# Performance work log

Hardware: AMD Instinct MI355X
Metric: run time of the kernel (lower is better)

Reference implementation:

```python
import jax, jax.numpy as jnp
import numpy as np
from jax import lax

NPOINT = 1024
K = 32
EPS = 1e-5  # BatchNorm eps (eval mode, running stats)


def _fps(xyz, npoint):
    """Farthest point sampling. xyz: [B,N,3] -> idx [B,npoint] (int32).
    Deterministic start at index 0 (torch version starts at a random index)."""
    B, N, _ = xyz.shape
    barange = jnp.arange(B)

    def step(carry, _):
        distance, farthest = carry
        centroid = xyz[barange, farthest]                    # [B,3]
        d = jnp.sum((xyz - centroid[:, None, :]) ** 2, -1)   # [B,N]
        distance = jnp.minimum(distance, d)
        new_far = jnp.argmax(distance, axis=-1).astype(jnp.int32)
        return (distance, new_far), farthest

    init = (jnp.full((B, N), 1e10, dtype=xyz.dtype), jnp.zeros((B,), jnp.int32))
    _, centroids = lax.scan(step, init, None, length=npoint)  # [npoint,B]
    return centroids.T                                        # [B,npoint]


def _square_distance(src, dst):
    # src [B,M,3], dst [B,N,3] -> [B,M,N]
    return (jnp.sum(src ** 2, -1)[:, :, None]
            - 2.0 * jnp.einsum('bmc,bnc->bmn', src, dst)
            + jnp.sum(dst ** 2, -1)[:, None, :])


def _gather(p, idx):
    # p [B,N,C], idx [B,...] -> [B,...,C]
    return jax.vmap(lambda pb, ib: pb[ib])(p, idx)


def _mlp_layer(x, w, cb, g, b, m, v):
    # x [B,S,K,Cin]; Conv2d 1x1 == channel matmul, then eval-mode BN, ReLU
    x = jnp.einsum('bskc,oc->bsko', x, w) + cb
    x = (x - m) * (g / jnp.sqrt(v + EPS)) + b
    return jax.nn.relu(x)


def _forward(xyz, points, w0, cb0, g0, b0, m0, v0,
             w1, cb1, g1, b1, m1, v1, w2, cb2, g2, b2, m2, v2):
    fps_idx = _fps(xyz, NPOINT)                       # [B,S]
    new_xyz = _gather(xyz, fps_idx)                   # [B,S,3]
    dists = _square_distance(new_xyz, xyz)            # [B,S,N]
    _, nn_idx = lax.top_k(-dists, K)                  # [B,S,K]
    grouped_xyz = _gather(xyz, nn_idx)                # [B,S,K,3]
    grouped_xyz_norm = grouped_xyz - new_xyz[:, :, None, :]
    grouped_pts = _gather(points, nn_idx)             # [B,S,K,C]
    x = jnp.concatenate([grouped_xyz_norm, grouped_pts], axis=-1)  # [B,S,K,3+C]
    x = _mlp_layer(x, w0, cb0, g0, b0, m0, v0)
    x = _mlp_layer(x, w1, cb1, g1, b1, m1, v1)
    x = _mlp_layer(x, w2, cb2, g2, b2, m2, v2)
    new_points = jnp.max(x, axis=2)                   # max over K -> [B,S,Cout]
    return new_xyz, jnp.transpose(new_points, (0, 2, 1))  # [B,Cout,S]


def setup_inputs() -> dict:
    key = jax.random.key(0)
    ks = jax.random.split(key, 8)
    B, N, C = 16, 4096, 64
    inp = {
        'xyz': jax.random.normal(ks[0], (B, N, 3), jnp.float32),
        'points': jax.random.normal(ks[1], (B, N, C), jnp.float32),
    }
    channels = [(3 + C, 64), (64, 64), (64, 128)]
    for li, (ci, co) in enumerate(channels):
        inp[f'w{li}'] = jax.random.normal(ks[2 + li], (co, ci), jnp.float32) * 0.05
        inp[f'cb{li}'] = jnp.zeros((co,), jnp.float32)
        inp[f'g{li}'] = jnp.ones((co,), jnp.float32)
        inp[f'b{li}'] = jnp.zeros((co,), jnp.float32)
        inp[f'm{li}'] = jnp.zeros((co,), jnp.float32)
        inp[f'v{li}'] = jnp.ones((co,), jnp.float32)
    return inp


def reference(xyz, points, w0, cb0, g0, b0, m0, v0,
              w1, cb1, g1, b1, m1, v1, w2, cb2, g2, b2, m2, v2):
    return _forward(xyz, points, w0, cb0, g0, b0, m0, v0,
                    w1, cb1, g1, b1, m1, v1, w2, cb2, g2, b2, m2, v2)
```

## Files before the change

### kernel.cpp

```cpp
#include <hip/hip_runtime.h>
#include <math.h>

#pragma clang fp contract(off)

#define NPTS 4096
#define NB 16
#define NS 1024
#define KNB 32
#define CPTS 64

#define FLAG_OFF_B  0
#define CNT_OFF_B   64
#define PUBC_OFF_B  128
#define WFRAG_ELEMS 18432
#define NUNITS      16384
#define CAP         256
#define GRAB        2

typedef __attribute__((ext_vector_type(8))) short short8;
typedef __attribute__((ext_vector_type(4))) float f32x4;
typedef __attribute__((ext_vector_type(2))) float f32x2;

__device__ __forceinline__ short f2bf(float f) {
  unsigned u = __float_as_uint(f);
  unsigned r = (u + 0x7fffu + ((u >> 16) & 1u)) >> 16;
  return (short)r;
}

template <int CTRL>
__device__ __forceinline__ int dppmov(int cur) {
  return __builtin_amdgcn_update_dpp(cur, cur, CTRL, 0xF, 0xF, false);
}
template <int CTRL>
__device__ __forceinline__ double dpp_fmax64(double x) {
  int hi = __double2hiint(x), lo = __double2loint(x);
  double o = __hiloint2double(dppmov<CTRL>(hi), dppmov<CTRL>(lo));
  return fmax(x, o);
}
__device__ __forceinline__ double mkkey(float d, unsigned lo) {
  return __hiloint2double((int)__float_as_uint(d), (int)lo);
}

#define XSTR 104
__global__ __launch_bounds__(512, 1) void fused_kernel(
    const float* __restrict__ xyz, const float* __restrict__ points,
    const float* __restrict__ w0, const float* __restrict__ cb0, const float* __restrict__ g0,
    const float* __restrict__ b0, const float* __restrict__ m0, const float* __restrict__ v0,
    const float* __restrict__ w1, const float* __restrict__ cb1, const float* __restrict__ g1,
    const float* __restrict__ b1, const float* __restrict__ m1, const float* __restrict__ v1,
    const float* __restrict__ w2, const float* __restrict__ cb2, const float* __restrict__ g2,
    const float* __restrict__ b2, const float* __restrict__ m2, const float* __restrict__ v2,
    char* __restrict__ wsb, float* __restrict__ newxyz, float* __restrict__ outp) {
  struct FpsSh {
    float4 sxyz4[NPTS];
    float4 centL[NS];
    unsigned long long part[2][8];
  };
  struct WorkerSh {
    short Wlds[WFRAG_ELEMS];
    short X[8][32 * XSTR];
    unsigned long long cand[8][CAP];
    int nnL[8][KNB];
    float biasL[256];
    unsigned cnt[8];
  };
  __shared__ union { FpsSh f; WorkerSh w; } sh;

  const int t = threadIdx.x;
  const int lane = t & 63;
  const int wave = t >> 6;
  unsigned* flagp = (unsigned*)(wsb + FLAG_OFF_B);
  unsigned* cntp  = (unsigned*)(wsb + CNT_OFF_B);
  float* pubC = (float*)(wsb + PUBC_OFF_B);

  if (blockIdx.x < NB) {
    const int b = blockIdx.x;
    const float* xb = xyz + (size_t)b * NPTS * 3;
    float* outb = newxyz + (size_t)b * NS * 3;

    for (int i = t; i < NPTS; i += 512)
      sh.f.sxyz4[i] = make_float4(xb[i * 3 + 0], xb[i * 3 + 1], xb[i * 3 + 2], 0.f);

    f32x2 px2[8], py2[8], pz2[8], d2[8];
    unsigned lo16[16];
    if (wave < 4) {
#pragma unroll
      for (int j = 0; j < 16; ++j) lo16[j] = ~(unsigned)(t + 256 * j);
#pragma unroll
      for (int j2 = 0; j2 < 8; ++j2) {
        int n0 = t + 512 * j2, n1 = t + 512 * j2 + 256;
        px2[j2].x = xb[n0 * 3 + 0]; px2[j2].y = xb[n1 * 3 + 0];
        py2[j2].x = xb[n0 * 3 + 1]; py2[j2].y = xb[n1 * 3 + 1];
        pz2[j2].x = xb[n0 * 3 + 2]; pz2[j2].y = xb[n1 * 3 + 2];
        d2[j2].x = 1e10f; d2[j2].y = 1e10f;
      }
    }
    __syncthreads();
    float cx = sh.f.sxyz4[0].x, cy = sh.f.sxyz4[0].y, cz = sh.f.sxyz4[0].z;
    if (t == 0) sh.f.centL[0] = sh.f.sxyz4[0];

    for (int it = 1; it < NS; ++it) {
      const int buf = it & 1;
      if (wave < 4) {
        f32x2 cax; cax.x = cx; cax.y = cx;
        f32x2 cay; cay.x = cy; cay.y = cy;
        f32x2 caz; caz.x = cz; caz.y = cz;
        double tt[8];
#pragma unroll
        for (int j2 = 0; j2 < 8; ++j2) {
          f32x2 dx = px2[j2] - cax;
          f32x2 dy = py2[j2] - cay;
          f32x2 dz = pz2[j2] - caz;
          f32x2 dd = (dx * dx + dy * dy) + dz * dz;
          f32x2 dv = d2[j2];
          dv.x = fminf(dv.x, dd.x);
          dv.y = fminf(dv.y, dd.y);
          d2[j2] = dv;
          tt[j2] = fmax(mkkey(dv.x, lo16[2 * j2]), mkkey(dv.y, lo16[2 * j2 + 1]));
        }
        double km = fmax(fmax(fmax(tt[0], tt[1]), fmax(tt[2], tt[3])),
                         fmax(fmax(tt[4], tt[5]), fmax(tt[6], tt[7])));
        km = dpp_fmax64<0xB1>(km);  km = dpp_fmax64<0x4E>(km);  km = dpp_fmax64<0x141>(km);
        km = dpp_fmax64<0x140>(km); km = dpp_fmax64<0x142>(km); km = dpp_fmax64<0x143>(km);
        if (lane == 63)
          sh.f.part[buf][wave] = (unsigned long long)__double_as_longlong(km);
      }
      __syncthreads();
      if (wave < 4) {
        double kw = __longlong_as_double((long long)sh.f.part[buf][lane & 3]);
        kw = dpp_fmax64<0xB1>(kw); kw = dpp_fmax64<0x4E>(kw);
        int bi = (int)(~(unsigned)__double2loint(kw)) & 4095;
        float4 c4 = sh.f.sxyz4[bi];
        cx = c4.x; cy = c4.y; cz = c4.z;
        if (t == 0) sh.f.centL[it] = c4;
        if ((it & 31) == 31 && wave == 0) {
          if (lane == 0) {
            asm volatile("s_waitcnt vmcnt(0)" ::: "memory");
            __hip_atomic_store(&flagp[b], (unsigned)(it - 31), __ATOMIC_RELAXED, __HIP_MEMORY_SCOPE_AGENT);
          }
          if (lane < 32) {
            int ci = it - 31 + lane;
            float4 cc = sh.f.centL[ci];
            float* dst = pubC + ((size_t)b * NS + ci) * 3;
            __hip_atomic_store(dst + 0, cc.x, __ATOMIC_RELAXED, __HIP_MEMORY_SCOPE_AGENT);
            __hip_atomic_store(dst + 1, cc.y, __ATOMIC_RELAXED, __HIP_MEMORY_SCOPE_AGENT);
            __hip_atomic_store(dst + 2, cc.z, __ATOMIC_RELAXED, __HIP_MEMORY_SCOPE_AGENT);
          }
        }
      }
    }
    if (wave == 0 && lane == 0) {
      asm volatile("s_waitcnt vmcnt(0)" ::: "memory");
      __hip_atomic_store(&flagp[b], (unsigned)NS, __ATOMIC_RELAXED, __HIP_MEMORY_SCOPE_AGENT);
    }
    __syncthreads();
    const float* cf = (const float*)sh.f.centL;
    for (int i = t; i < NS * 3; i += 512) {
      int p = i / 3, c = i - p * 3;
      outb[i] = cf[p * 4 + c];
    }
  }

  __syncthreads();
  for (int i = t; i < WFRAG_ELEMS; i += 512) {
    int g = i >> 9, ln = (i >> 3) & 63, j = i & 7;
    int l, nt, s;
    if (g < 12)      { l = 0; nt = g / 3;  s = g % 3; }
    else if (g < 20) { l = 1; int gg = g - 12; nt = gg >> 1; s = gg & 1; }
    else             { l = 2; int gg = g - 20; nt = gg >> 1; s = gg & 1; }
    int n = nt * 16 + (ln & 15);
    int k = s * 32 + ((ln >> 4) << 3) + j;
    float val = 0.f;
    if (l == 0) {
      float sc = g0[n] / sqrtf(v0[n] + 1e-5f);
      if (k < 64)      val = w0[n * 67 + (k + 3)] * sc;
      else if (k < 67) val = w0[n * 67 + (k - 64)] * sc;
    }
    else if (l == 1) { val = w1[n * 64 + k] * (g1[n] / sqrtf(v1[n] + 1e-5f)); }
    else { val = w2[n * 64 + k] * (g2[n] / sqrtf(v2[n] + 1e-5f)); }
    sh.w.Wlds[i] = f2bf(val);
  }
  if (t < 256) {
    int o = t;
    float bv;
    if (o < 64)       { float sc = g0[o] / sqrtf(v0[o] + 1e-5f); bv = (cb0[o] - m0[o]) * sc + b0[o]; }
    else if (o < 128) { int c = o - 64;  float sc = g1[c] / sqrtf(v1[c] + 1e-5f); bv = (cb1[c] - m1[c]) * sc + b1[c]; }
    else              { int c = o - 128; float sc = g2[c] / sqrtf(v2[c] + 1e-5f); bv = (cb2[c] - m2[c]) * sc + b2[c]; }
    sh.w.biasL[o] = bv;
  }
  __syncthreads();

  unsigned long long* cand = sh.w.cand[wave];
  for (int i = lane; i < (32 * XSTR) / 2; i += 64) ((int*)sh.w.X[wave])[i] = 0;

  unsigned fcache = 0;

  for (;;) {
    unsigned base = 0;
    if (lane == 0) base = atomicAdd(cntp, (unsigned)GRAB);
    base = (unsigned)__builtin_amdgcn_readfirstlane((int)base);
    if (base >= NUNITS) break;
    unsigned uend = base + GRAB;
    if (uend > NUNITS) uend = NUNITS;

    for (unsigned u = base; u < uend; ++u) {
    const int b = (int)(u & 15u);
    const int s = (int)(u >> 4);

    {
      unsigned need = (unsigned)s + 1u;
      unsigned have = (unsigned)__shfl((int)fcache, b, 64);
      if (have < need) {
        unsigned f;
        for (;;) {
          f = __hip_atomic_load(&flagp[b], __ATOMIC_RELAXED, __HIP_MEMORY_SCOPE_AGENT);
          if (f >= need) break;
          __builtin_amdgcn_s_sleep(64);
        }
        if (lane == b) fcache = f;
        asm volatile("" ::: "memory");
      }
    }
    const float* qcp = pubC + ((size_t)b * NS + s) * 3;
    float qx = __hip_atomic_load(qcp + 0, __ATOMIC_RELAXED, __HIP_MEMORY_SCOPE_AGENT);
    float qy = __hip_atomic_load(qcp + 1, __ATOMIC_RELAXED, __HIP_MEMORY_SCOPE_AGENT);
    float qz = __hip_atomic_load(qcp + 2, __ATOMIC_RELAXED, __HIP_MEMORY_SCOPE_AGENT);

    const float* xb = xyz + (size_t)b * NPTS * 3;
    float s2 = __fadd_rn(__fadd_rn(__fmul_rn(qx, qx), __fmul_rn(qy, qy)), __fmul_rn(qz, qz));

    unsigned long long mkey = 0xFFFFFFFFFFFFFFFFull;
#pragma unroll 4
    for (int j = 0; j < 64; ++j) {
      int n = j * 64 + lane;
      float px = xb[n * 3], py = xb[n * 3 + 1], pz = xb[n * 3 + 2];
      float n2 = __fadd_rn(__fadd_rn(__fmul_rn(px, px), __fmul_rn(py, py)), __fmul_rn(pz, pz));
      float dt = __fadd_rn(__fadd_rn(__fmul_rn(qx, px), __fmul_rn(qy, py)), __fmul_rn(qz, pz));
      float d  = __fadd_rn(__fsub_rn(s2, __fmul_rn(2.0f, dt)), n2);
      unsigned uu = __float_as_uint(d);
      uu ^= (0x80000000u | (unsigned)((int)uu >> 31));
      unsigned long long key = ((unsigned long long)uu << 32) | (unsigned)n;
      mkey = key < mkey ? key : mkey;
    }

    {
      unsigned mh = (unsigned)(mkey >> 32), ml2 = (unsigned)mkey;
#pragma unroll
      for (int k = 2; k <= 64; k <<= 1) {
#pragma unroll
        for (int j = k >> 1; j >= 1; j >>= 1) {
          unsigned oh = (unsigned)__shfl_xor((int)mh, j, 64);
          unsigned ol = (unsigned)__shfl_xor((int)ml2, j, 64);
          bool up = (lane & k) == 0;
          bool lower = (lane & j) == 0;
          bool omin = (oh < mh) || (oh == mh && ol < ml2);
          bool keep_o = (lower == up) ? omin : !omin;
          mh = keep_o ? oh : mh;
          ml2 = keep_o ? ol : ml2;
        }
      }
      unsigned th = (unsigned)__builtin_amdgcn_readlane((int)mh, 31);
      unsigned tl = (unsigned)__builtin_amdgcn_readlane((int)ml2, 31);
      mkey = ((unsigned long long)th << 32) | tl;
    }
    const unsigned long long tau = mkey;

    if (lane == 0) sh.w.cnt[wave] = 0;
    asm volatile("s_waitcnt lgkmcnt(0)" ::: "memory");
#pragma unroll 4
    for (int j = 0; j < 64; ++j) {
      int n = j * 64 + lane;
      float px = xb[n * 3], py = xb[n * 3 + 1], pz = xb[n * 3 + 2];
      float n2 = __fadd_rn(__fadd_rn(__fmul_rn(px, px), __fmul_rn(py, py)), __fmul_rn(pz, pz));
      float dt = __fadd_rn(__fadd_rn(__fmul_rn(qx, px), __fmul_rn(qy, py)), __fmul_rn(qz, pz));
      float d  = __fadd_rn(__fsub_rn(s2, __fmul_rn(2.0f, dt)), n2);
      unsigned uu = __float_as_uint(d);
      uu ^= (0x80000000u | (unsigned)((int)uu >> 31));
      unsigned long long key = ((unsigned long long)uu << 32) | (unsigned)n;
      if (key <= tau) {
        unsigned pos = atomicAdd(&sh.w.cnt[wave], 1u);
        if (pos < CAP) cand[pos] = key;
      }
    }
    asm volatile("s_waitcnt lgkmcnt(0)" ::: "memory");
    unsigned cn = sh.w.cnt[wave];
    if (cn > CAP) cn = CAP;

    for (unsigned bb = 0; bb < cn; bb += 64) {
      unsigned i = bb + (unsigned)lane;
      unsigned long long ki = (i < cn) ? cand[i] : 0xFFFFFFFFFFFFFFFFull;
      int rank = 0;
#pragma unroll 4
      for (unsigned c2 = 0; c2 < cn; ++c2)
        rank += (cand[c2] < ki) ? 1 : 0;
      if (i < cn && rank < KNB) sh.w.nnL[wave][rank] = (int)(unsigned)(ki & 0xFFFFFFFFull);
    }
    asm volatile("s_waitcnt lgkmcnt(0)" ::: "memory");

    {
      const int qi = wave;
      const float* pb = points + (size_t)b * NPTS * CPTS;
      const float* bias = sh.w.biasL;
      short* X = sh.w.X[qi];

      {
        int h = lane & 1, r = lane >> 1;
        int idx = sh.w.nnL[qi][r];
        const f32x4* src = (const f32x4*)(pb + (size_t)idx * CPTS) + h * 8;
        short8* dst = (short8*)&X[r * XSTR + h * 32];
#pragma unroll
        for (int q = 0; q < 4; ++q) {
          f32x4 v0 = src[q * 2], v1 = src[q * 2 + 1];
          short8 o;
          o[0] = f2bf(v0[0]); o[1] = f2bf(v0[1]); o[2] = f2bf(v0[2]); o[3] = f2bf(v0[3]);
          o[4] = f2bf(v1[0]); o[5] = f2bf(v1[1]); o[6] = f2bf(v1[2]); o[7] = f2bf(v1[3]);
          dst[q] = o;
        }
      }
      if (lane < 32) {
        int idx = sh.w.nnL[qi][lane];
        X[lane * XSTR + 64] = f2bf(__fsub_rn(xb[idx * 3 + 0], qx));
        X[lane * XSTR + 65] = f2bf(__fsub_rn(xb[idx * 3 + 1], qy));
        X[lane * XSTR + 66] = f2bf(__fsub_rn(xb[idx * 3 + 2], qz));
      }

      const int ml = lane & 15, quad = lane >> 4;
      const short8* Wf = (const short8*)sh.w.Wlds;

      short8 a0[2][3];
#pragma unroll
      for (int m2 = 0; m2 < 2; ++m2)
#pragma unroll
        for (int s3 = 0; s3 < 3; ++s3)
          a0[m2][s3] = *(const short8*)&X[(m2 * 16 + ml) * XSTR + s3 * 32 + quad * 8];
      f32x4 acc0[2][4];
#pragma unroll
      for (int m2 = 0; m2 < 2; ++m2)
#pragma unroll
        for (int nt = 0; nt < 4; ++nt) {
          f32x4 c = {0.f, 0.f, 0.f, 0.f};
#pragma unroll
          for (int s3 = 0; s3 < 3; ++s3)
            c = __builtin_amdgcn_mfma_f32_16x16x32_bf16(a0[m2][s3], Wf[(nt * 3 + s3) * 64 + lane], c, 0, 0, 0);
          acc0[m2][nt] = c;
        }
#pragma unroll
      for (int m2 = 0; m2 < 2; ++m2)
#pragma unroll
        for (int nt = 0; nt < 4; ++nt) {
          int ch = nt * 16 + ml;
          float bv = bias[ch];
#pragma unroll
          for (int r4 = 0; r4 < 4; ++r4) {
            float y = fmaxf(acc0[m2][nt][r4] + bv, 0.f);
            int m = quad * 4 + r4;
            int sK = ch >> 5, qq = (ch >> 3) & 3, jj = ch & 7;
            X[((m2 * 2 + sK) * 64 + qq * 16 + m) * 8 + jj] = f2bf(y);
          }
        }

      short8 a1[2][2];
#pragma unroll
      for (int m2 = 0; m2 < 2; ++m2)
#pragma unroll
        for (int sK = 0; sK < 2; ++sK)
          a1[m2][sK] = *(const short8*)&X[((m2 * 2 + sK) * 64 + lane) * 8];
      f32x4 acc1[2][4];
#pragma unroll
      for (int m2 = 0; m2 < 2; ++m2)
#pragma unroll
        for (int nt = 0; nt < 4; ++nt) {
          f32x4 c = {0.f, 0.f, 0.f, 0.f};
#pragma unroll
          for (int sK = 0; sK < 2; ++sK)
            c = __builtin_amdgcn_mfma_f32_16x16x32_bf16(a1[m2][sK], Wf[(12 + nt * 2 + sK) * 64 + lane], c, 0, 0, 0);
          acc1[m2][nt] = c;
        }
#pragma unroll
      for (int m2 = 0; m2 < 2; ++m2)
#pragma unroll
        for (int nt = 0; nt < 4; ++nt) {
          int ch = nt * 16 + ml;
          float bv = bias[64 + ch];
#pragma unroll
          for (int r4 = 0; r4 < 4; ++r4) {
            float y = fmaxf(acc1[m2][nt][r4] + bv, 0.f);
            int m = quad * 4 + r4;
            int sK = ch >> 5, qq = (ch >> 3) & 3, jj = ch & 7;
            X[((m2 * 2 + sK) * 64 + qq * 16 + m) * 8 + jj] = f2bf(y);
          }
        }

      short8 a2[2][2];
#pragma unroll
      for (int m2 = 0; m2 < 2; ++m2)
#pragma unroll
        for (int sK = 0; sK < 2; ++sK)
          a2[m2][sK] = *(const short8*)&X[((m2 * 2 + sK) * 64 + lane) * 8];
#pragma unroll
      for (int nt = 0; nt < 8; ++nt) {
        f32x4 c0 = {0.f, 0.f, 0.f, 0.f}, c1 = {0.f, 0.f, 0.f, 0.f};
        short8 w0f = Wf[(20 + nt * 2 + 0) * 64 + lane];
        short8 w1f = Wf[(20 + nt * 2 + 1) * 64 + lane];
        c0 = __builtin_amdgcn_mfma_f32_16x16x32_bf16(a2[0][0], w0f, c0, 0, 0, 0);
        c0 = __builtin_amdgcn_mfma_f32_16x16x32_bf16(a2[0][1], w1f, c0, 0, 0, 0);
        c1 = __builtin_amdgcn_mfma_f32_16x16x32_bf16(a2[1][0], w0f, c1, 0, 0, 0);
        c1 = __builtin_amdgcn_mfma_f32_16x16x32_bf16(a2[1][1], w1f, c1, 0, 0, 0);
        float bv = bias[128 + nt * 16 + ml];
        float m = -1.f;
#pragma unroll
        for (int r4 = 0; r4 < 4; ++r4) {
          m = fmaxf(m, fmaxf(c0[r4] + bv, 0.f));
          m = fmaxf(m, fmaxf(c1[r4] + bv, 0.f));
        }
        m = fmaxf(m, __shfl_xor(m, 16, 64));
        m = fmaxf(m, __shfl_xor(m, 32, 64));
        if (lane < 16) outp[((size_t)b * 128 + nt * 16 + lane) * NS + s] = m;
      }
    }
    }
  }
}

extern "C" void kernel_launch(void* const* d_in, const int* in_sizes, int n_in,
                              void* d_out, int out_size, void* d_ws, size_t ws_size,
                              hipStream_t stream) {
  const float* xyz    = (const float*)d_in[0];
  const float* points = (const float*)d_in[1];
  const float* w0  = (const float*)d_in[2];
  const float* cb0 = (const float*)d_in[3];
  const float* g0  = (const float*)d_in[4];
  const float* b0  = (const float*)d_in[5];
  const float* m0  = (const float*)d_in[6];
  const float* v0  = (const float*)d_in[7];
  const float* w1  = (const float*)d_in[8];
  const float* cb1 = (const float*)d_in[9];
  const float* g1  = (const float*)d_in[10];
  const float* b1  = (const float*)d_in[11];
  const float* m1  = (const float*)d_in[12];
  const float* v1  = (const float*)d_in[13];
  const float* w2  = (const float*)d_in[14];
  const float* cb2 = (const float*)d_in[15];
  const float* g2  = (const float*)d_in[16];
  const float* b2  = (const float*)d_in[17];
  const float* m2  = (const float*)d_in[18];
  const float* v2  = (const float*)d_in[19];

  char*  wsb    = (char*)d_ws;
  float* newxyz = (float*)d_out;
  float* outp   = (float*)d_out + (size_t)NB * NS * 3;

  hipMemsetAsync(wsb, 0, 128, stream);
  fused_kernel<<<256, 512, 0, stream>>>(
      xyz, points, w0, cb0, g0, b0, m0, v0, w1, cb1, g1, b1, m1, v1,
      w2, cb2, g2, b2, m2, v2, wsb, newxyz, outp);
}
```

Before: 901.8 us.

## Pack two FPS batch chains per block and relax launch bounds to two blocks

```diff
diff --git a/kernel.cpp b/kernel.cpp
--- a/kernel.cpp
+++ b/kernel.cpp
@@ -16,6 +16,7 @@
 #define NUNITS      16384
 #define CAP         256
 #define GRAB        2
+#define NFPSB       8
 
 typedef __attribute__((ext_vector_type(8))) short short8;
 typedef __attribute__((ext_vector_type(4))) float f32x4;
@@ -42,7 +43,7 @@
 }
 
 #define XSTR 104
-__global__ __launch_bounds__(512, 1) void fused_kernel(
+__global__ __launch_bounds__(512, 2) void fused_kernel(
     const float* __restrict__ xyz, const float* __restrict__ points,
     const float* __restrict__ w0, const float* __restrict__ cb0, const float* __restrict__ g0,
     const float* __restrict__ b0, const float* __restrict__ m0, const float* __restrict__ v0,
@@ -52,8 +53,8 @@
     const float* __restrict__ b2, const float* __restrict__ m2, const float* __restrict__ v2,
     char* __restrict__ wsb, float* __restrict__ newxyz, float* __restrict__ outp) {
   struct FpsSh {
-    float4 sxyz4[NPTS];
-    float4 centL[NS];
+    float4 sxyz4[2][NPTS];
+    float  centL[2][NS * 3];
     unsigned long long part[2][8];
   };
   struct WorkerSh {
@@ -73,91 +74,92 @@
   unsigned* cntp  = (unsigned*)(wsb + CNT_OFF_B);
   float* pubC = (float*)(wsb + PUBC_OFF_B);
 
-  if (blockIdx.x < NB) {
-    const int b = blockIdx.x;
+  if (blockIdx.x < NFPSB) {
+    const int chain = wave >> 2;
+    const int wc = wave & 3;
+    const int tc = wc * 64 + lane;
+    const int b = (int)blockIdx.x * 2 + chain;
     const float* xb = xyz + (size_t)b * NPTS * 3;
-    float* outb = newxyz + (size_t)b * NS * 3;
-
-    for (int i = t; i < NPTS; i += 512)
-      sh.f.sxyz4[i] = make_float4(xb[i * 3 + 0], xb[i * 3 + 1], xb[i * 3 + 2], 0.f);
+    float4* sx = sh.f.sxyz4[chain];
+    float* cL = sh.f.centL[chain];
+
+    for (int i = tc; i < NPTS; i += 256)
+      sx[i] = make_float4(xb[i * 3 + 0], xb[i * 3 + 1], xb[i * 3 + 2], 0.f);
 
     f32x2 px2[8], py2[8], pz2[8], d2[8];
     unsigned lo16[16];
-    if (wave < 4) {
-#pragma unroll
-      for (int j = 0; j < 16; ++j) lo16[j] = ~(unsigned)(t + 256 * j);
-#pragma unroll
-      for (int j2 = 0; j2 < 8; ++j2) {
-        int n0 = t + 512 * j2, n1 = t + 512 * j2 + 256;
-        px2[j2].x = xb[n0 * 3 + 0]; px2[j2].y = xb[n1 * 3 + 0];
-        py2[j2].x = xb[n0 * 3 + 1]; py2[j2].y = xb[n1 * 3 + 1];
-        pz2[j2].x = xb[n0 * 3 + 2]; pz2[j2].y = xb[n1 * 3 + 2];
-        d2[j2].x = 1e10f; d2[j2].y = 1e10f;
-      }
+#pragma unroll
+    for (int j = 0; j < 16; ++j) lo16[j] = ~(unsigned)(tc + 256 * j);
+#pragma unroll
+    for (int j2 = 0; j2 < 8; ++j2) {
+      int n0 = tc + 512 * j2, n1 = n0 + 256;
+      px2[j2].x = xb[n0 * 3 + 0]; px2[j2].y = xb[n1 * 3 + 0];
+      py2[j2].x = xb[n0 * 3 + 1]; py2[j2].y = xb[n1 * 3 + 1];
+      pz2[j2].x = xb[n0 * 3 + 2]; pz2[j2].y = xb[n1 * 3 + 2];
+      d2[j2].x = 1e10f; d2[j2].y = 1e10f;
     }
     __syncthreads();
-    float cx = sh.f.sxyz4[0].x, cy = sh.f.sxyz4[0].y, cz = sh.f.sxyz4[0].z;
-    if (t == 0) sh.f.centL[0] = sh.f.sxyz4[0];
+    float4 c4 = sx[0];
+    float cx = c4.x, cy = c4.y, cz = c4.z;
+    if (wc == 0 && lane == 0) { cL[0] = cx; cL[1] = cy; cL[2] = cz; }
 
     for (int it = 1; it < NS; ++it) {
       const int buf = it & 1;
-      if (wave < 4) {
-        f32x2 cax; cax.x = cx; cax.y = cx;
-        f32x2 cay; cay.x = cy; cay.y = cy;
-        f32x2 caz; caz.x = cz; caz.y = cz;
-        double tt[8];
-#pragma unroll
-        for (int j2 = 0; j2 < 8; ++j2) {
-          f32x2 dx = px2[j2] - cax;
-          f32x2 dy = py2[j2] - cay;
-          f32x2 dz = pz2[j2] - caz;
-          f32x2 dd = (dx * dx + dy * dy) + dz * dz;
-          f32x2 dv = d2[j2];
-          dv.x = fminf(dv.x, dd.x);
-          dv.y = fminf(dv.y, dd.y);
-          d2[j2] = dv;
-          tt[j2] = fmax(mkkey(dv.x, lo16[2 * j2]), mkkey(dv.y, lo16[2 * j2 + 1]));
-        }
-        double km = fmax(fmax(fmax(tt[0], tt[1]), fmax(tt[2], tt[3])),
-                         fmax(fmax(tt[4], tt[5]), fmax(tt[6], tt[7])));
-        km = dpp_fmax64<0xB1>(km);  km = dpp_fmax64<0x4E>(km);  km = dpp_fmax64<0x141>(km);
-        km = dpp_fmax64<0x140>(km); km = dpp_fmax64<0x142>(km); km = dpp_fmax64<0x143>(km);
-        if (lane == 63)
-          sh.f.part[buf][wave] = (unsigned long long)__double_as_longlong(km);
-      }
+      f32x2 cax; cax.x = cx; cax.y = cx;
+      f32x2 cay; cay.x = cy; cay.y = cy;
+      f32x2 caz; caz.x = cz; caz.y = cz;
+      double tt[8];
+#pragma unroll
+      for (int j2 = 0; j2 < 8; ++j2) {
+        f32x2 dx = px2[j2] - cax;
+        f32x2 dy = py2[j2] - cay;
+        f32x2 dz = pz2[j2] - caz;
+        f32x2 dd = (dx * dx + dy * dy) + dz * dz;
+        f32x2 dv = d2[j2];
+        dv.x = fminf(dv.x, dd.x);
+        dv.y = fminf(dv.y, dd.y);
+        d2[j2] = dv;
+        tt[j2] = fmax(mkkey(dv.x, lo16[2 * j2]), mkkey(dv.y, lo16[2 * j2 + 1]));
+      }
+      double km = fmax(fmax(fmax(tt[0], tt[1]), fmax(tt[2], tt[3])),
+                       fmax(fmax(tt[4], tt[5]), fmax(tt[6], tt[7])));
+      km = dpp_fmax64<0xB1>(km);  km = dpp_fmax64<0x4E>(km);  km = dpp_fmax64<0x141>(km);
+      km = dpp_fmax64<0x140>(km); km = dpp_fmax64<0x142>(km); km = dpp_fmax64<0x143>(km);
+      if (lane == 63)
+        sh.f.part[buf][wave] = (unsigned long long)__double_as_longlong(km);
       __syncthreads();
-      if (wave < 4) {
-        double kw = __longlong_as_double((long long)sh.f.part[buf][lane & 3]);
-        kw = dpp_fmax64<0xB1>(kw); kw = dpp_fmax64<0x4E>(kw);
-        int bi = (int)(~(unsigned)__double2loint(kw)) & 4095;
-        float4 c4 = sh.f.sxyz4[bi];
-        cx = c4.x; cy = c4.y; cz = c4.z;
-        if (t == 0) sh.f.centL[it] = c4;
-        if ((it & 31) == 31 && wave == 0) {
-          if (lane == 0) {
-            asm volatile("s_waitcnt vmcnt(0)" ::: "memory");
-            __hip_atomic_store(&flagp[b], (unsigned)(it - 31), __ATOMIC_RELAXED, __HIP_MEMORY_SCOPE_AGENT);
-          }
-          if (lane < 32) {
-            int ci = it - 31 + lane;
-            float4 cc = sh.f.centL[ci];
-            float* dst = pubC + ((size_t)b * NS + ci) * 3;
-            __hip_atomic_store(dst + 0, cc.x, __ATOMIC_RELAXED, __HIP_MEMORY_SCOPE_AGENT);
-            __hip_atomic_store(dst + 1, cc.y, __ATOMIC_RELAXED, __HIP_MEMORY_SCOPE_AGENT);
-            __hip_atomic_store(dst + 2, cc.z, __ATOMIC_RELAXED, __HIP_MEMORY_SCOPE_AGENT);
-          }
-        }
-      }
-    }
-    if (wave == 0 && lane == 0) {
+      double kw = __longlong_as_double(
+          (long long)sh.f.part[buf][chain * 4 + (lane & 3)]);
+      kw = dpp_fmax64<0xB1>(kw); kw = dpp_fmax64<0x4E>(kw);
+      int bi = (int)(~(unsigned)__double2loint(kw)) & 4095;
+      float4 cc = sx[bi];
+      cx = cc.x; cy = cc.y; cz = cc.z;
+      if (wc == 0 && lane == 0) {
+        cL[it * 3 + 0] = cx; cL[it * 3 + 1] = cy; cL[it * 3 + 2] = cz;
+      }
+      if ((it & 31) == 31 && wc == 0) {
+        if (lane == 0) {
+          asm volatile("s_waitcnt vmcnt(0)" ::: "memory");
+          __hip_atomic_store(&flagp[b], (unsigned)(it - 31), __ATOMIC_RELAXED, __HIP_MEMORY_SCOPE_AGENT);
+        }
+        if (lane < 32) {
+          int ci = it - 31 + lane;
+          float x = cL[ci * 3 + 0], y = cL[ci * 3 + 1], z = cL[ci * 3 + 2];
+          float* dst = pubC + ((size_t)b * NS + ci) * 3;
+          __hip_atomic_store(dst + 0, x, __ATOMIC_RELAXED, __HIP_MEMORY_SCOPE_AGENT);
+          __hip_atomic_store(dst + 1, y, __ATOMIC_RELAXED, __HIP_MEMORY_SCOPE_AGENT);
+          __hip_atomic_store(dst + 2, z, __ATOMIC_RELAXED, __HIP_MEMORY_SCOPE_AGENT);
+        }
+      }
+    }
+    if (wc == 0 && lane == 0) {
       asm volatile("s_waitcnt vmcnt(0)" ::: "memory");
       __hip_atomic_store(&flagp[b], (unsigned)NS, __ATOMIC_RELAXED, __HIP_MEMORY_SCOPE_AGENT);
     }
     __syncthreads();
-    const float* cf = (const float*)sh.f.centL;
-    for (int i = t; i < NS * 3; i += 512) {
-      int p = i / 3, c = i - p * 3;
-      outb[i] = cf[p * 4 + c];
+    {
+      float* outb = newxyz + (size_t)b * NS * 3;
+      for (int i = tc; i < NS * 3; i += 256) outb[i] = cL[i];
     }
   }
 
```

Result: slower. 1.044 ms (+15.8%).
